# Optimization experiments

Measured on AMD Instinct MI355X. Metric: run time of the kernel, lower is better.

## Reference

```python
import jax, jax.numpy as jnp
import numpy as np

I, H, M, C, LOC, K = 512, 256, 80, 1024, 32, 31
C2 = C // 2
B, S, T = 32, 256, 800


def setup_inputs() -> dict:
    key = jax.random.key(0)
    ks = jax.random.split(key, 20)
    sc = 0.02
    return {
        "encodings": jax.random.normal(ks[0], (B, S, I), jnp.float32),
        "queries": jax.random.normal(ks[1], (B, T, H), jnp.float32),
        "outputs": jax.random.normal(ks[2], (B, T, M), jnp.float32),
        "mask": jnp.ones((B, S), jnp.float32),
        # GRUCell (PyTorch layout: gates ordered r, z, n)
        "w_ih": jax.random.normal(ks[3], (3 * C, I + H), jnp.float32) * sc,
        "w_hh": jax.random.normal(ks[4], (3 * C, C), jnp.float32) * sc,
        "b_ih": jax.random.normal(ks[5], (3 * C,), jnp.float32) * sc,
        "b_hh": jax.random.normal(ks[6], (3 * C,), jnp.float32) * sc,
        "w_q": jax.random.normal(ks[7], (C2, C), jnp.float32) * sc,        # proj_query
        "w_loc1": jax.random.normal(ks[8], (LOC, 1, K), jnp.float32) * sc, # Conv1d(1, loc, K)
        "w_loc2": jax.random.normal(ks[9], (C2, LOC), jnp.float32) * sc,   # Conv1d(loc, C2, 1)
        "w_k": jax.random.normal(ks[10], (C2, I), jnp.float32) * sc,       # proj_key
        "b_k": jax.random.normal(ks[11], (C2,), jnp.float32) * sc,
        "w_agg": jax.random.normal(ks[12], (C2,), jnp.float32) * sc,       # Conv1d(C2, 1, 1)
        "w_t1": jax.random.normal(ks[13], (C, I + C + M), jnp.float32) * sc,
        "b_t1": jax.random.normal(ks[14], (C,), jnp.float32) * sc,
        "w_t2": jax.random.normal(ks[15], (C,), jnp.float32) * sc,
    }


def _conv1d(x, w, pad):
    # x: [B, Cin, S], w: [Cout, Cin, K]
    return jax.lax.conv_general_dilated(
        x, w, window_strides=(1,), padding=[(pad, pad)],
        dimension_numbers=("NCH", "OIH", "NCH"))


def _aligner(encodings, queries, outputs, maskb,
             w_ih, w_hh, b_ih, b_hh, w_q, w_loc1, w_loc2, w_k, b_k,
             w_agg, w_t1, b_t1, w_t2):
    bsize, seqlen, _ = encodings.shape
    # key projection: [B, S, C2]
    key = encodings @ w_k.T + b_k
    h0 = jnp.zeros((bsize, C), encodings.dtype)
    align0 = jnp.full((bsize, seqlen), 1.0 / seqlen, encodings.dtype)
    alpha0 = jnp.zeros((bsize, seqlen), encodings.dtype).at[:, 0].set(1.0)
    trans0 = jnp.full((bsize, 1), 0.5, encodings.dtype)

    def step(carry, xt):
        h, align, trans, alpha = carry
        query, frame = xt  # [B,H], [B,M]
        prev = jnp.einsum("bsi,bs->bi", encodings, alpha)
        x = jnp.concatenate([query, prev], axis=-1)  # [B, H+I]
        gx = x @ w_ih.T + b_ih
        gh = h @ w_hh.T + b_hh
        xr, xz, xn = jnp.split(gx, 3, axis=-1)
        hr, hz, hn = jnp.split(gh, 3, axis=-1)
        r = jax.nn.sigmoid(xr + hr)
        z = jax.nn.sigmoid(xz + hz)
        n = jnp.tanh(xn + r * hn)
        h_new = (1.0 - z) * n + z * h  # GRUCell update
        # location features: [B,1,S] -> [B,LOC,S] -> [B,C2,S]
        loc = _conv1d(align[:, None, :], w_loc1, K // 2)
        loc = jnp.einsum("cl,bls->bcs", w_loc2, loc)
        score = loc + (h_new @ w_q.T)[..., None] + key.swapaxes(1, 2)  # [B,C2,S]
        energy = jnp.einsum("c,bcs->bs", w_agg, jnp.tanh(score))
        energy = jnp.where(maskb, -jnp.inf, energy)
        align_new = jax.nn.softmax(energy, axis=-1)
        shifted = jnp.pad(alpha, ((0, 0), (1, 0)))[:, :-1]  # F.pad(alpha, [1,-1])
        alpha_new = ((1.0 - trans) * alpha + trans * shifted + 1e-7) * align_new
        alpha_new = alpha_new / alpha_new.sum(axis=-1, keepdims=True)
        attend = jnp.einsum("bsi,bs->bi", encodings, alpha_new)
        t_in = jnp.concatenate([attend, frame, h_new], axis=-1)
        t = jax.nn.sigmoid(jnp.tanh(t_in @ w_t1.T + b_t1) @ w_t2[:, None])  # [B,1]
        return (h_new, align_new, t, alpha_new), alpha_new

    xs = (queries.swapaxes(0, 1), outputs.swapaxes(0, 1))
    _, alphas = jax.lax.scan(step, (h0, align0, trans0, alpha0), xs)
    return alphas.swapaxes(0, 1)  # [B, T, S]


def reference(encodings, queries, outputs, mask,
              w_ih, w_hh, b_ih, b_hh, w_q, w_loc1, w_loc2, w_k, b_k,
              w_agg, w_t1, b_t1, w_t2):
    maskb = ~(mask.astype(bool))
    return _aligner(encodings, queries, outputs, maskb,
                    w_ih, w_hh, b_ih, b_hh, w_q, w_loc1, w_loc2, w_k, b_k,
                    w_agg, w_t1, b_t1, w_t2)
```

## Files before the change

kernel.cpp:

```cpp
#include <hip/hip_runtime.h>
#include <cstdint>
#include <cstddef>


namespace cfg {
constexpr int NB = 32, NS = 256, NI = 512, NHq = 256, NM = 80;
constexpr int NC = 1024, NC2 = 512, NT = 800;
constexpr int NBLK = 256, NTHR = 512;

constexpr size_t OFF_KEYT  = 0;
constexpr size_t OFF_WKT   = OFF_KEYT + (size_t)NB * NS * NC2;
constexpr size_t OFF_PU    = OFF_WKT + (size_t)NI * NC2;
constexpr size_t OFF_H     = OFF_PU + (size_t)2 * NB * NI;
constexpr size_t OFF_H16   = OFF_H + (size_t)2 * NC * NB;
constexpr size_t OFF_E     = OFF_H16 + (size_t)NB * NC;
constexpr size_t OFF_W     = OFF_E + (size_t)2 * NB * NS;
constexpr size_t OFF_SE    = OFF_W + (size_t)2 * NB * NS;
constexpr size_t OFF_SW    = OFF_SE + 64;
constexpr size_t OFF_TPART = OFF_SW + 64;
constexpr size_t OFF_TRED  = OFF_TPART + (size_t)NB * NBLK;
constexpr size_t OFF_QBUF  = OFF_TRED + 32;
constexpr size_t OFF_BAR   = OFF_QBUF + (size_t)NB * NC2;
constexpr size_t OFF_Q16   = OFF_BAR + 8192;
constexpr size_t OFF_F16   = OFF_Q16 + (size_t)NT * NB * NHq / 2;
constexpr size_t OFF_WQ16  = OFF_F16 + (size_t)NT * NB * 128 / 2;
constexpr size_t OFF_ENC16 = OFF_WQ16 + (size_t)NC2 * NC / 2;
constexpr size_t WS_FLOATS = OFF_ENC16 + (size_t)NB * NS * NI / 2;
}
using namespace cfg;

typedef __attribute__((ext_vector_type(8))) short short8;
typedef __attribute__((ext_vector_type(4))) float f32x4;

#define MF(a, b, c) __builtin_amdgcn_mfma_f32_16x16x32_bf16((a), (b), (c), 0, 0, 0)
#define LDSC(d, p) asm volatile("global_load_dwordx4 %0, %1, off sc0 sc1" : "=v"(d) : "v"(p))

__device__ __forceinline__ float ld_cg(const float* p) {
  return __hip_atomic_load(p, __ATOMIC_RELAXED, __HIP_MEMORY_SCOPE_AGENT);
}
__device__ __forceinline__ void st_cg(float* p, float v) {
  __hip_atomic_store(p, v, __ATOMIC_RELAXED, __HIP_MEMORY_SCOPE_AGENT);
}
__device__ __forceinline__ void st_cg_u16(unsigned short* p, unsigned short v) {
  asm volatile("global_store_short %0, %1, off sc0 sc1" :: "v"(p), "v"((unsigned)v) : "memory");
}

__device__ __forceinline__ void vw7(short8& a0, short8& a1, short8& a2, short8& a3,
                                    short8& a4, short8& a5, short8& a6) {
  asm volatile("s_waitcnt vmcnt(0)"
               : "+v"(a0), "+v"(a1), "+v"(a2), "+v"(a3), "+v"(a4), "+v"(a5), "+v"(a6));
}
__device__ __forceinline__ void vw8(short8& a0, short8& a1, short8& a2, short8& a3,
                                    short8& a4, short8& a5, short8& a6, short8& a7) {
  asm volatile("s_waitcnt vmcnt(0)"
               : "+v"(a0), "+v"(a1), "+v"(a2), "+v"(a3), "+v"(a4), "+v"(a5), "+v"(a6), "+v"(a7));
}
__device__ __forceinline__ void vw10(short8& a0, short8& a1, short8& a2, short8& a3, short8& a4,
                                     short8& a5, short8& a6, short8& a7, short8& a8, short8& a9) {
  asm volatile("s_waitcnt vmcnt(0)"
               : "+v"(a0), "+v"(a1), "+v"(a2), "+v"(a3), "+v"(a4), "+v"(a5), "+v"(a6),
                 "+v"(a7), "+v"(a8), "+v"(a9));
}
__device__ __forceinline__ void vw15(short8& a0, short8& a1, short8& a2, short8& a3, short8& a4,
                                     short8& a5, short8& a6, short8& a7, short8& a8, short8& a9,
                                     short8& aa, short8& ab2, short8& ac, short8& ad, short8& ae) {
  asm volatile("s_waitcnt vmcnt(0)"
               : "+v"(a0), "+v"(a1), "+v"(a2), "+v"(a3), "+v"(a4), "+v"(a5), "+v"(a6),
                 "+v"(a7), "+v"(a8), "+v"(a9), "+v"(aa), "+v"(ab2), "+v"(ac), "+v"(ad), "+v"(ae));
}
__device__ __forceinline__ void vw16f(f32x4& a0, f32x4& a1, f32x4& a2, f32x4& a3, f32x4& a4,
                                      f32x4& a5, f32x4& a6, f32x4& a7, f32x4& b0, f32x4& b1,
                                      f32x4& b2, f32x4& b3, f32x4& b4, f32x4& b5, f32x4& b6,
                                      f32x4& b7) {
  asm volatile("s_waitcnt vmcnt(0)"
               : "+v"(a0), "+v"(a1), "+v"(a2), "+v"(a3), "+v"(a4), "+v"(a5), "+v"(a6), "+v"(a7),
                 "+v"(b0), "+v"(b1), "+v"(b2), "+v"(b3), "+v"(b4), "+v"(b5), "+v"(b6), "+v"(b7));
}

__device__ __forceinline__ float frcp(float x) {
#if __has_builtin(__builtin_amdgcn_rcpf)
  return __builtin_amdgcn_rcpf(x);
#else
  return 1.f / x;
#endif
}
__device__ __forceinline__ float fsig(float x) { return frcp(1.f + __expf(-x)); }
__device__ __forceinline__ float ftanh(float x) {
  const float e = __expf(2.f * x);
  return 1.f - 2.f * frcp(e + 1.f);
}
__device__ __forceinline__ short f2bf(float f) {
  unsigned u = __float_as_uint(f);
  u += 0x7FFFu + ((u >> 16) & 1u);
  return (short)(u >> 16);
}
__device__ __forceinline__ float bfu(unsigned short u) {
  return __uint_as_float(((unsigned)u) << 16);
}
__device__ __forceinline__ short8 cvt8(f32x4 lo, f32x4 hi) {
  short8 a;
  a[0] = f2bf(lo[0]); a[1] = f2bf(lo[1]); a[2] = f2bf(lo[2]); a[3] = f2bf(lo[3]);
  a[4] = f2bf(hi[0]); a[5] = f2bf(hi[1]); a[6] = f2bf(hi[2]); a[7] = f2bf(hi[3]);
  return a;
}

__device__ __forceinline__ void gbarrier(unsigned* root, unsigned* flags, unsigned& ph) {
  ++ph;
  asm volatile("s_waitcnt vmcnt(0)" ::: "memory");
  __syncthreads();
  unsigned* rootrep = root + 4352;
  if (blockIdx.x == 0) {
    const int t = threadIdx.x;
    if (t > 0 && t < 256) {
      while (__hip_atomic_load(&flags[t * 16], __ATOMIC_RELAXED, __HIP_MEMORY_SCOPE_AGENT) < ph)
        __builtin_amdgcn_s_sleep(1);
    }
    __syncthreads();
    if (t < 32)
      __hip_atomic_store(&rootrep[t * 16], ph, __ATOMIC_RELAXED, __HIP_MEMORY_SCOPE_AGENT);
  } else {
    if (threadIdx.x == 0) {
      __hip_atomic_store(&flags[blockIdx.x * 16], ph, __ATOMIC_RELAXED, __HIP_MEMORY_SCOPE_AGENT);
      while (__hip_atomic_load(&rootrep[(blockIdx.x & 31) * 16], __ATOMIC_RELAXED,
                               __HIP_MEMORY_SCOPE_AGENT) < ph)
        __builtin_amdgcn_s_sleep(1);
    }
  }
  __syncthreads();
}

__device__ __forceinline__ float wcat_val(const float* __restrict__ w_ih,
                                          const float* __restrict__ w_hh,
                                          const float* __restrict__ w_t1,
                                          int kind, int c, int k) {
  if (kind < 3) {
    const int gr = kind * NC + c;
    if (k < 768) return w_ih[(size_t)gr * 768 + k];
    if (k < 1792) return w_hh[(size_t)gr * NC + (k - 768)];
    return 0.f;
  }
  if (k >= 256 && k < 768) return w_t1[(size_t)c * 1616 + (k - 256)];
  if (k >= 768 && k < 1792) return w_t1[(size_t)c * 1616 + 592 + (k - 768)];
  if (k >= 1792 && k < 1872) return w_t1[(size_t)c * 1616 + 512 + (k - 1792)];
  return 0.f;
}

__global__ void k_init(const float* __restrict__ enc, const float* __restrict__ queries,
                       const float* __restrict__ outputs, const float* __restrict__ w_k,
                       const float* __restrict__ w_q, float* __restrict__ ws) {
  const size_t t0 = (size_t)blockIdx.x * blockDim.x + threadIdx.x;
  const size_t gs = (size_t)gridDim.x * blockDim.x;
  for (size_t x = t0; x < (size_t)NI * NC2; x += gs) {
    const int i = (int)(x / NC2), c2 = (int)(x % NC2);
    ws[OFF_WKT + x] = w_k[(size_t)c2 * NI + i];
  }
  for (size_t x = t0; x < (size_t)NB * NI; x += gs) {
    const int b = (int)(x / NI), i = (int)(x % NI);
    ws[OFF_PU + x] = 0.f;
    ws[OFF_PU + (size_t)NB * NI + b * NI + i] = enc[(size_t)b * NS * NI + i];
  }
  for (size_t x = t0; x < (size_t)2 * NC * NB; x += gs) ws[OFF_H + x] = 0.f;
  for (size_t x = t0; x < (size_t)NB * NC; x += gs) ws[OFF_H16 + x] = 0.f;
  for (size_t x = t0; x < (size_t)NB * NS; x += gs) {
    ws[OFF_E + x] = 0.f;
    ws[OFF_E + (size_t)NB * NS + x] = 1.f;
    ws[OFF_W + x] = 0.f;
    ws[OFF_W + (size_t)NB * NS + x] = ((x & (NS - 1)) == 0) ? 1.f : 0.f;
  }
  for (size_t x = t0; x < (size_t)NB; x += gs) {
    ws[OFF_SE + x] = 0.f; ws[OFF_SE + NB + x] = (float)NS;
    ws[OFF_SW + x] = 0.f; ws[OFF_SW + NB + x] = 1.f;
    ws[OFF_TRED + x] = 0.f;
  }
  for (size_t x = t0; x < (size_t)NB * NBLK; x += gs) ws[OFF_TPART + x] = 0.f;
  unsigned* bar = (unsigned*)(ws + OFF_BAR);
  for (size_t x = t0; x < 8192; x += gs) bar[x] = 0u;
  unsigned short* Q16 = (unsigned short*)(ws + OFF_Q16);
  for (size_t x = t0; x < (size_t)NT * NB * NHq; x += gs) {
    const int k = (int)(x & (NHq - 1));
    const int b = (int)((x >> 8) & (NB - 1));
    const int t = (int)(x >> 13);
    Q16[x] = (unsigned short)f2bf(queries[((size_t)b * NT + t) * NHq + k]);
  }
  unsigned short* F16 = (unsigned short*)(ws + OFF_F16);
  for (size_t x = t0; x < (size_t)NT * NB * 128; x += gs) {
    const int k = (int)(x & 127);
    const int b = (int)((x >> 7) & (NB - 1));
    const int t = (int)(x >> 12);
    F16[x] = (k < NM) ? (unsigned short)f2bf(outputs[((size_t)b * NT + t) * NM + k]) : 0;
  }
  unsigned short* WQ16 = (unsigned short*)(ws + OFF_WQ16);
  for (size_t x = t0; x < (size_t)NC2 * NC; x += gs)
    WQ16[x] = (unsigned short)f2bf(w_q[x]);
  unsigned short* ENC16 = (unsigned short*)(ws + OFF_ENC16);
  for (size_t x = t0; x < (size_t)NB * NS * NI; x += gs)
    ENC16[x] = (unsigned short)f2bf(enc[x]);
}

__global__ __launch_bounds__(NTHR) void k_key(const float* __restrict__ enc,
                                              const float* __restrict__ b_k,
                                              float* __restrict__ ws) {
  __shared__ float encl[4 * NI];
  const int bid = blockIdx.x, tid = threadIdx.x;
  const int b = bid >> 3, s0 = (bid & 7) * 32;
  const float* wkT = ws + OFF_WKT;
  float* keyT = ws + OFF_KEYT;
  const float bk = b_k[tid];
  for (int q = 0; q < 8; ++q) {
    const int sb = s0 + q * 4;
    for (int x = tid; x < 4 * NI; x += NTHR) {
      const int ss = x >> 9, i = x & (NI - 1);
      encl[x] = enc[((size_t)(b * NS + sb + ss)) * NI + i];
    }
    __syncthreads();
    float a0 = bk, a1 = bk, a2 = bk, a3 = bk;
    for (int i = 0; i < NI; ++i) {
      const float wv = wkT[(size_t)i * NC2 + tid];
      a0 += wv * encl[i];           a1 += wv * encl[NI + i];
      a2 += wv * encl[2 * NI + i];  a3 += wv * encl[3 * NI + i];
    }
    keyT[((size_t)(b * NS + sb + 0)) * NC2 + tid] = a0;
    keyT[((size_t)(b * NS + sb + 1)) * NC2 + tid] = a1;
    keyT[((size_t)(b * NS + sb + 2)) * NC2 + tid] = a2;
    keyT[((size_t)(b * NS + sb + 3)) * NC2 + tid] = a3;
    __syncthreads();
  }
}

__global__ __launch_bounds__(NTHR, 2) void k_main(
    const float* __restrict__ enc, const float* __restrict__ mask,
    const float* __restrict__ w_ih, const float* __restrict__ w_hh,
    const float* __restrict__ b_ih, const float* __restrict__ b_hh,
    const float* __restrict__ w_loc1, const float* __restrict__ w_loc2,
    const float* __restrict__ w_agg, const float* __restrict__ w_t1,
    const float* __restrict__ b_t1, const float* __restrict__ w_t2,
    float* ws, float* __restrict__ out) {
  const int bid = blockIdx.x, tid = threadIdx.x;
  float* const keyT = ws + OFF_KEYT;
  float* const PU = ws + OFF_PU;
  float* const HB = ws + OFF_H;
  unsigned short* const HB16 = (unsigned short*)(ws + OFF_H16);
  float* const EB = ws + OFF_E;
  float* const WBUF = ws + OFF_W;
  float* const SEB = ws + OFF_SE;
  float* const SWB = ws + OFF_SW;
  float* const TPART = ws + OFF_TPART;
  float* const QBUF = ws + OFF_QBUF;
  unsigned* const root = (unsigned*)(ws + OFF_BAR);
  unsigned* const flags = root + 16;
  unsigned* const qflag = root + 5120;
  unsigned* const rootrep2 = root + 5632;
  const unsigned short* const Q16 = (const unsigned short*)(ws + OFF_Q16);
  const unsigned short* const F16 = (const unsigned short*)(ws + OFF_F16);
  const unsigned short* const WQ16 = (const unsigned short*)(ws + OFF_WQ16);
  const unsigned short* const ENC16 = (const unsigned short*)(ws + OFF_ENC16);

  __shared__ float Cred[2 * 5 * 4 * 64];
  __shared__ float gout2[5 * 4 * 32];
  __shared__ float swinv_l[32];
  __shared__ float tredl[128];
  __shared__ float redT[256];
  __shared__ float alignl[72];
  __shared__ float wl2[34];
  __shared__ float qbl[520];
  __shared__ float Epart[32 * 9];
  __shared__ float wstash[32];
  __shared__ float scal[4];

  const int lane = tid & 63, wv = tid >> 6;
  const int m2 = wv >> 2, k4 = wv & 3;
  const int kg = lane >> 4;
  const int ab = m2 * 16 + (lane & 15);
  const int cs = bid * 4;
  const int pb_b = bid >> 3, pb_s0 = (bid & 7) * 32;
  const int col = lane & 15, quad = lane >> 4;
  unsigned ph = 0;

  short8 wreg[16];
  {
    const int n = lane & 15;
    const int kind = n >> 2, ch = cs + (n & 3);
#pragma unroll
    for (int si = 0; si < 16; ++si) {
      int s = (k4 == 0) ? (si < 8 ? si : (si < 15 ? 16 + si : -1))
            : (k4 == 1) ? 8 + si
            : (k4 == 2) ? (si < 15 ? 31 + si : -1)
                        : (si < 14 ? 46 + si : -1);
      short8 w = {0, 0, 0, 0, 0, 0, 0, 0};
      if (s >= 0) {
        const int k0 = s * 32 + kg * 8;
#pragma unroll
        for (int jj = 0; jj < 8; ++jj)
          w[jj] = f2bf(wcat_val(w_ih, w_hh, w_t1, kind, ch, k0 + jj));
      }
      wreg[si] = w;
    }
  }
  short8 wcA[4];
  unsigned keylo[4][2], keyhi[4][2];
  f32x4 wagr[4];
#pragma unroll
  for (int t = 0; t < 4; ++t) {
    const int mt = 4 * wv + t;
    short8 wfr;
#pragma unroll
    for (int jj = 0; jj < 8; ++jj) {
      const int k = quad * 8 + jj;
      float s = 0.f;
      if (k < 31) {
        const int c2 = mt * 16 + col;
        for (int l = 0; l < 32; ++l) s += w_loc2[c2 * 32 + l] * w_loc1[l * 31 + k];
      }
      wfr[jj] = f2bf(s);
    }
    wcA[t] = wfr;
    const int c2r = mt * 16 + quad * 4;
#pragma unroll
    for (int r = 0; r < 4; ++r) wagr[t][r] = w_agg[c2r + r];
#pragma unroll
    for (int nt = 0; nt < 2; ++nt) {
      const float* kp = &keyT[((size_t)(pb_b * NS + pb_s0 + nt * 16 + col)) * NC2 + c2r];
      keylo[t][nt] = ((unsigned)(unsigned short)f2bf(kp[0])) |
                     (((unsigned)(unsigned short)f2bf(kp[1])) << 16);
      keyhi[t][nt] = ((unsigned)(unsigned short)f2bf(kp[2])) |
                     (((unsigned)(unsigned short)f2bf(kp[3])) << 16);
    }
  }
  if (tid >= 62 && tid < 72) alignl[tid] = 0.f;
  __syncthreads();

  for (int j = 0; j < NT; ++j) {
    const int p = j & 1;
    const float* pu_prev = PU + (size_t)(1 - p) * NB * NI;
    float* pu_cur = PU + (size_t)p * NB * NI;
    const float* h_prev = HB + (size_t)(1 - p) * NC * NB;
    float* h_cur = HB + (size_t)p * NC * NB;
    const unsigned short* hb16_prev = HB16 + (size_t)(1 - p) * NB * NC;
    unsigned short* hb16_cur = HB16 + (size_t)p * NB * NC;
    const float* e_prev = EB + (size_t)(1 - p) * NB * NS;
    float* e_cur = EB + (size_t)p * NB * NS;
    const float* w_prev = WBUF + (size_t)(1 - p) * NB * NS;
    float* w_cur = WBUF + (size_t)p * NB * NS;
    const float* se_prev = SEB + (size_t)(1 - p) * NB;
    float* se_cur = SEB + (size_t)p * NB;
    const float* sw_prev = SWB + (size_t)(1 - p) * NB;
    float* sw_cur = SWB + (size_t)p * NB;

    if (tid < 64) st_cg(&pu_cur[bid * 64 + tid], 0.f);
    if (bid == 0 && tid < NB) st_cg(&se_cur[tid], 0.f);
    if (bid == 1 && tid < NB) st_cg(&sw_cur[tid], 0.f);
    if (tid < NB) swinv_l[tid] = 1.f / ld_cg(&sw_prev[tid]);
    if (tid == 0) scal[0] = ld_cg(&se_prev[pb_b]);
    if (tid < 62) {
      const int sp = pb_s0 + tid - 15;
      alignl[tid] = (sp >= 0 && sp < NS) ? ld_cg(&e_prev[pb_b * NS + sp]) : 0.f;
    }
    if (tid >= 64 && tid < 97) {
      const int i2 = tid - 64, sp = pb_s0 + i2 - 1;
      wl2[i2] = (sp >= 0 && sp < NS) ? ld_cg(&w_prev[pb_b * NS + sp]) : 0.f;
    }
    __syncthreads();

    if (j >= 1 && bid < NB && tid < NS)
      out[((size_t)bid * NT + (j - 1)) * NS + tid] = ld_cg(&w_prev[bid * NS + tid]) * swinv_l[bid];

    f32x4 accA = {0.f, 0.f, 0.f, 0.f}, accB = {0.f, 0.f, 0.f, 0.f};
    if (k4 == 0) {
      const unsigned short* qp = Q16 + ((size_t)j * NB + ab) * NHq + kg * 8;
      const unsigned short* hp = hb16_prev + (size_t)ab * NC + kg * 8;
      short8 h0, h1, h2, h3, h4, h5, h6;
      LDSC(h0, hp);        LDSC(h1, hp + 32);   LDSC(h2, hp + 64);  LDSC(h3, hp + 96);
      LDSC(h4, hp + 128);  LDSC(h5, hp + 160);  LDSC(h6, hp + 192);
      const short8 q0 = *(const short8*)(qp);
      const short8 q1 = *(const short8*)(qp + 32);
      const short8 q2 = *(const short8*)(qp + 64);
      const short8 q3 = *(const short8*)(qp + 96);
      const short8 q4 = *(const short8*)(qp + 128);
      const short8 q5 = *(const short8*)(qp + 160);
      const short8 q6 = *(const short8*)(qp + 192);
      const short8 q7 = *(const short8*)(qp + 224);
      vw7(h0, h1, h2, h3, h4, h5, h6);
      accA = MF(q0, wreg[0], accA); accA = MF(q1, wreg[1], accA);
      accA = MF(q2, wreg[2], accA); accA = MF(q3, wreg[3], accA);
      accA = MF(q4, wreg[4], accA); accA = MF(q5, wreg[5], accA);
      accA = MF(q6, wreg[6], accA); accA = MF(q7, wreg[7], accA);
      accB = MF(h0, wreg[8], accB);  accB = MF(h1, wreg[9], accB);
      accB = MF(h2, wreg[10], accB); accB = MF(h3, wreg[11], accB);
      accB = MF(h4, wreg[12], accB); accB = MF(h5, wreg[13], accB);
      accB = MF(h6, wreg[14], accB);
    } else if (k4 == 1) {
      const float* pp = pu_prev + (size_t)ab * NI + kg * 8;
#pragma unroll
      for (int rd = 0; rd < 2; ++rd) {
        const float* pb = pp + rd * 256;
        f32x4 a0, a1, a2, a3, a4, a5, a6, a7, b0, b1, b2, b3, b4, b5, b6, b7;
        LDSC(a0, pb);        LDSC(b0, pb + 4);
        LDSC(a1, pb + 32);   LDSC(b1, pb + 36);
        LDSC(a2, pb + 64);   LDSC(b2, pb + 68);
        LDSC(a3, pb + 96);   LDSC(b3, pb + 100);
        LDSC(a4, pb + 128);  LDSC(b4, pb + 132);
        LDSC(a5, pb + 160);  LDSC(b5, pb + 164);
        LDSC(a6, pb + 192);  LDSC(b6, pb + 196);
        LDSC(a7, pb + 224);  LDSC(b7, pb + 228);
        vw16f(a0, a1, a2, a3, a4, a5, a6, a7, b0, b1, b2, b3, b4, b5, b6, b7);
        const int w0 = rd * 8;
        accA = MF(cvt8(a0, b0), wreg[w0 + 0], accA);
        accA = MF(cvt8(a1, b1), wreg[w0 + 1], accA);
        accA = MF(cvt8(a2, b2), wreg[w0 + 2], accA);
        accA = MF(cvt8(a3, b3), wreg[w0 + 3], accA);
        accA = MF(cvt8(a4, b4), wreg[w0 + 4], accA);
        accA = MF(cvt8(a5, b5), wreg[w0 + 5], accA);
        accA = MF(cvt8(a6, b6), wreg[w0 + 6], accA);
        accA = MF(cvt8(a7, b7), wreg[w0 + 7], accA);
      }
    } else if (k4 == 2) {
      const unsigned short* hp = hb16_prev + (size_t)ab * NC + kg * 8 + 224;
      short8 h0, h1, h2, h3, h4, h5, h6, h7, h8, h9, ha, hb2, hc, hd, he;
      LDSC(h0, hp);        LDSC(h1, hp + 32);  LDSC(h2, hp + 64);  LDSC(h3, hp + 96);
      LDSC(h4, hp + 128);  LDSC(h5, hp + 160); LDSC(h6, hp + 192); LDSC(h7, hp + 224);
      LDSC(h8, hp + 256);  LDSC(h9, hp + 288); LDSC(ha, hp + 320); LDSC(hb2, hp + 352);
      LDSC(hc, hp + 384);  LDSC(hd, hp + 416); LDSC(he, hp + 448);
      vw15(h0, h1, h2, h3, h4, h5, h6, h7, h8, h9, ha, hb2, hc, hd, he);
      accA = MF(h0, wreg[0], accA);  accA = MF(h1, wreg[1], accA);
      accA = MF(h2, wreg[2], accA);  accA = MF(h3, wreg[3], accA);
      accA = MF(h4, wreg[4], accA);  accA = MF(h5, wreg[5], accA);
      accA = MF(h6, wreg[6], accA);  accA = MF(h7, wreg[7], accA);
      accA = MF(h8, wreg[8], accA);  accA = MF(h9, wreg[9], accA);
      accA = MF(ha, wreg[10], accA); accA = MF(hb2, wreg[11], accA);
      accA = MF(hc, wreg[12], accA); accA = MF(hd, wreg[13], accA);
      accA = MF(he, wreg[14], accA);
    } else {
      const unsigned short* hp = hb16_prev + (size_t)ab * NC + kg * 8 + 704;
      short8 h0, h1, h2, h3, h4, h5, h6, h7, h8, h9;
      LDSC(h0, hp);        LDSC(h1, hp + 32);  LDSC(h2, hp + 64);  LDSC(h3, hp + 96);
      LDSC(h4, hp + 128);  LDSC(h5, hp + 160); LDSC(h6, hp + 192); LDSC(h7, hp + 224);
      LDSC(h8, hp + 256);  LDSC(h9, hp + 288);
      short8 f0 = {0,0,0,0,0,0,0,0}, f1 = f0, f2 = f0, f3 = f0;
      if (j > 0) {
        const unsigned short* fp = F16 + ((size_t)(j - 1) * NB + ab) * 128 + kg * 8;
        f0 = *(const short8*)(fp);
        f1 = *(const short8*)(fp + 32);
        f2 = *(const short8*)(fp + 64);
        f3 = *(const short8*)(fp + 96);
      }
      vw10(h0, h1, h2, h3, h4, h5, h6, h7, h8, h9);
      accA = MF(h0, wreg[0], accA); accA = MF(h1, wreg[1], accA);
      accA = MF(h2, wreg[2], accA); accA = MF(h3, wreg[3], accA);
      accA = MF(h4, wreg[4], accA); accA = MF(h5, wreg[5], accA);
      accA = MF(h6, wreg[6], accA); accA = MF(h7, wreg[7], accA);
      accA = MF(h8, wreg[8], accA); accA = MF(h9, wreg[9], accA);
      accA = MF(f0, wreg[10], accA); accA = MF(f1, wreg[11], accA);
      accA = MF(f2, wreg[12], accA); accA = MF(f3, wreg[13], accA);
    }
    {
      auto cidx = [](int m, int sg, int r, int l) { return ((m * 5 + sg) * 4 + r) * 64 + l; };
      if (k4 == 0) {
#pragma unroll
        for (int r = 0; r < 4; ++r) {
          Cred[cidx(m2, 0, r, lane)] = accA[r];
          Cred[cidx(m2, 1, r, lane)] = accB[r];
        }
      } else {
        const int sg = 1 + k4;
#pragma unroll
        for (int r = 0; r < 4; ++r) Cred[cidx(m2, sg, r, lane)] = accA[r];
      }
    }
    __syncthreads();
    {
      const int n = tid & 15, b = tid >> 4;
      const int m2r = b >> 4, bm = b & 15, l = (bm >> 2) * 16 + n, r = bm & 3;
      auto cidx = [](int m, int sg, int rr, int ll) { return ((m * 5 + sg) * 4 + rr) * 64 + ll; };
      const float s0 = Cred[cidx(m2r, 0, r, l)];
      const float sB = Cred[cidx(m2r, 1, r, l)];
      const float s1 = Cred[cidx(m2r, 2, r, l)];
      const float s2 = sB + Cred[cidx(m2r, 3, r, l)] + Cred[cidx(m2r, 4, r, l)];
      const float swv = swinv_l[b];
      const int kind = n >> 2, c4o = n & 3;
      if (kind == 2) {
        gout2[2 * 128 + c4o * 32 + b] = s0 + swv * s1;
        gout2[3 * 128 + c4o * 32 + b] = s2;
      } else {
        const int slot = (kind == 3) ? 4 : kind;
        gout2[slot * 128 + c4o * 32 + b] = s0 + swv * s1 + s2;
      }
    }
    __syncthreads();
    if (tid < 128) {
      const int c4o = tid >> 5, b = tid & 31, c = cs + c4o;
      const float xr = gout2[0 * 128 + c4o * 32 + b] + b_ih[c] + b_hh[c];
      const float xz = gout2[1 * 128 + c4o * 32 + b] + b_ih[NC + c] + b_hh[NC + c];
      const float xn = gout2[2 * 128 + c4o * 32 + b] + b_ih[2 * NC + c];
      const float hn = gout2[3 * 128 + c4o * 32 + b] + b_hh[2 * NC + c];
      const float tp = gout2[4 * 128 + c4o * 32 + b];
      const float r = fsig(xr), z = fsig(xz);
      const float nn = ftanh(xn + r * hn);
      const float hnew = (1.f - z) * nn + z * h_prev[c * 32 + b];
      h_cur[c * 32 + b] = hnew;
      st_cg_u16(&hb16_cur[(size_t)b * NC + c], (unsigned short)f2bf(hnew));
      tredl[c4o * 32 + b] = w_t2[c] * ftanh(tp + b_t1[c]);
    }
    __syncthreads();
    if (tid < NB)
      st_cg(&TPART[(size_t)tid * NBLK + bid],
            tredl[tid] + tredl[32 + tid] + tredl[64 + tid] + tredl[96 + tid]);
    gbarrier(root, flags, ph);

    const float tpv = (tid < 256) ? ld_cg(&TPART[(size_t)pb_b * NBLK + tid]) : 0.f;

    if (bid < 32) {
      f32x4 qacc = {0.f, 0.f, 0.f, 0.f};
      const unsigned short* hb = hb16_cur + (size_t)ab * NC + kg * 8;
      short8 g0, g1, g2, g3, g4, g5, g6, g7;
      LDSC(g0, hb + (k4 * 8 + 0) * 32); LDSC(g1, hb + (k4 * 8 + 1) * 32);
      LDSC(g2, hb + (k4 * 8 + 2) * 32); LDSC(g3, hb + (k4 * 8 + 3) * 32);
      LDSC(g4, hb + (k4 * 8 + 4) * 32); LDSC(g5, hb + (k4 * 8 + 5) * 32);
      LDSC(g6, hb + (k4 * 8 + 6) * 32); LDSC(g7, hb + (k4 * 8 + 7) * 32);
      const int jq = bid * 16 + col;
      const unsigned short* wp = WQ16 + (size_t)jq * NC + k4 * 8 * 32 + kg * 8;
      vw8(g0, g1, g2, g3, g4, g5, g6, g7);
      qacc = MF(g0, *(const short8*)(wp), qacc);
      qacc = MF(g1, *(const short8*)(wp + 32), qacc);
      qacc = MF(g2, *(const short8*)(wp + 64), qacc);
      qacc = MF(g3, *(const short8*)(wp + 96), qacc);
      qacc = MF(g4, *(const short8*)(wp + 128), qacc);
      qacc = MF(g5, *(const short8*)(wp + 160), qacc);
      qacc = MF(g6, *(const short8*)(wp + 192), qacc);
      qacc = MF(g7, *(const short8*)(wp + 224), qacc);
#pragma unroll
      for (int r = 0; r < 4; ++r) Cred[((m2 * 4 + k4) * 4 + r) * 64 + lane] = qacc[r];
      __syncthreads();
      {
        const int col2 = tid & 15, b2 = tid >> 4;
        const int m2r = b2 >> 4, bm = b2 & 15, l = (bm >> 2) * 16 + col2, r = bm & 3;
        float s = 0.f;
#pragma unroll
        for (int kk = 0; kk < 4; ++kk) s += Cred[((m2r * 4 + kk) * 4 + r) * 64 + l];
        st_cg(&QBUF[(size_t)b2 * NC2 + bid * 16 + col2], s);
      }
      asm volatile("s_waitcnt vmcnt(0)" ::: "memory");
      __syncthreads();
      if (tid == 0)
        __hip_atomic_store(&qflag[bid * 16], (unsigned)(j + 1),
                           __ATOMIC_RELAXED, __HIP_MEMORY_SCOPE_AGENT);
    }

    if (tid < 256) redT[tid] = tpv;
    __syncthreads();
    if (tid < 64) {
      float s = redT[tid] + redT[tid + 64] + redT[tid + 128] + redT[tid + 192];
#pragma unroll
      for (int off = 32; off > 0; off >>= 1) s += __shfl_xor(s, off);
      if (tid == 0) scal[2] = s;
    }
    f32x4 bacc[2][4];
    {
      const float invSE = 1.f / scal[0];
#pragma unroll
      for (int nt = 0; nt < 2; ++nt) {
        const int base = nt * 16 + col + quad * 8;
        short8 bv;
#pragma unroll
        for (int jj = 0; jj < 8; ++jj) bv[jj] = f2bf(alignl[base + jj] * invSE);
#pragma unroll
        for (int t = 0; t < 4; ++t) {
          f32x4 acc;
          acc[0] = __uint_as_float(keylo[t][nt] << 16);
          acc[1] = __uint_as_float(keylo[t][nt] & 0xffff0000u);
          acc[2] = __uint_as_float(keyhi[t][nt] << 16);
          acc[3] = __uint_as_float(keyhi[t][nt] & 0xffff0000u);
          bacc[nt][t] = MF(wcA[t], bv, acc);
        }
      }
    }
    if (bid == 128) {
      if (tid < 32) {
        while (__hip_atomic_load(&qflag[tid * 16], __ATOMIC_RELAXED,
                                 __HIP_MEMORY_SCOPE_AGENT) < (unsigned)(j + 1))
          __builtin_amdgcn_s_sleep(1);
      }
      __syncthreads();
      if (tid < 32)
        __hip_atomic_store(&rootrep2[tid * 16], (unsigned)(j + 1),
                           __ATOMIC_RELAXED, __HIP_MEMORY_SCOPE_AGENT);
    } else {
      if (tid == 0) {
        while (__hip_atomic_load(&rootrep2[(bid & 31) * 16], __ATOMIC_RELAXED,
                                 __HIP_MEMORY_SCOPE_AGENT) < (unsigned)(j + 1))
          __builtin_amdgcn_s_sleep(1);
      }
    }
    __syncthreads();

    {
      const int b = pb_b, s0v = pb_s0;
      qbl[tid] = ld_cg(&QBUF[(size_t)b * NC2 + tid]);
      __syncthreads();
      const float invSW = swinv_l[b];
      const float tr = (j == 0) ? 0.5f : fsig(scal[2]);
#pragma unroll
      for (int nt = 0; nt < 2; ++nt) {
        float pe = 0.f;
#pragma unroll
        for (int t = 0; t < 4; ++t) {
          const int c2b = (4 * wv + t) * 16 + quad * 4;
          const f32x4 av = bacc[nt][t];
          pe += wagr[t][0] * ftanh(av[0] + qbl[c2b + 0]);
          pe += wagr[t][1] * ftanh(av[1] + qbl[c2b + 1]);
          pe += wagr[t][2] * ftanh(av[2] + qbl[c2b + 2]);
          pe += wagr[t][3] * ftanh(av[3] + qbl[c2b + 3]);
        }
        pe += __shfl_xor(pe, 16);
        pe += __shfl_xor(pe, 32);
        if (lane < 16) Epart[(nt * 16 + col) * 9 + wv] = pe;
      }
      __syncthreads();
      if (tid < 32) {
        const int sl = tid, s = s0v + sl;
        float Ev = 0.f;
#pragma unroll
        for (int w8 = 0; w8 < 8; ++w8) Ev += Epart[sl * 9 + w8];
        const float ev = (mask[b * NS + s] != 0.f) ? __expf(Ev) : 0.f;
        const float csv = ((1.f - tr) * wl2[sl + 1] + tr * wl2[sl]) * invSW + 1e-7f;
        const float wvv = csv * ev;
        st_cg(&e_cur[b * NS + s], ev);
        st_cg(&w_cur[b * NS + s], wvv);
        wstash[sl] = wvv;
        float se = ev, sw2 = wvv;
#pragma unroll
        for (int off = 16; off > 0; off >>= 1) {
          se += __shfl_down(se, off, 32);
          sw2 += __shfl_down(sw2, off, 32);
        }
        if (sl == 0) { atomicAdd(&se_cur[b], se); atomicAdd(&sw_cur[b], sw2); }
      }
      __syncthreads();
      {
        const unsigned short* ep = ENC16 + ((size_t)(b * NS + s0v)) * NI + tid;
        float acc = 0.f;
#pragma unroll 8
        for (int ss = 0; ss < 32; ++ss) acc += wstash[ss] * bfu(ep[(size_t)ss * NI]);
        atomicAdd(&pu_cur[(size_t)b * NI + tid], acc);
      }
    }
    gbarrier(root, flags, ph);
  }

  if (bid < NB && tid < NS) {
    const float invSW = 1.f / ld_cg(&SWB[NB + bid]);
    out[((size_t)bid * NT + (NT - 1)) * NS + tid] =
        ld_cg(&WBUF[(size_t)NB * NS + bid * NS + tid]) * invSW;
  }
}

extern "C" void kernel_launch(void* const* d_in, const int* in_sizes, int n_in,
                              void* d_out, int out_size, void* d_ws, size_t ws_size,
                              hipStream_t stream) {
  const float* enc     = (const float*)d_in[0];
  const float* queries = (const float*)d_in[1];
  const float* outputs = (const float*)d_in[2];
  const float* mask    = (const float*)d_in[3];
  const float* w_ih    = (const float*)d_in[4];
  const float* w_hh    = (const float*)d_in[5];
  const float* b_ih    = (const float*)d_in[6];
  const float* b_hh    = (const float*)d_in[7];
  const float* w_q     = (const float*)d_in[8];
  const float* w_loc1  = (const float*)d_in[9];
  const float* w_loc2  = (const float*)d_in[10];
  const float* w_k     = (const float*)d_in[11];
  const float* b_k     = (const float*)d_in[12];
  const float* w_agg   = (const float*)d_in[13];
  const float* w_t1    = (const float*)d_in[14];
  const float* b_t1    = (const float*)d_in[15];
  const float* w_t2    = (const float*)d_in[16];
  float* ws = (float*)d_ws;
  float* out = (float*)d_out;
  (void)in_sizes; (void)n_in; (void)out_size; (void)ws_size;

  k_init<<<dim3(1024), dim3(256), 0, stream>>>(enc, queries, outputs, w_k, w_q, ws);
  k_key<<<dim3(NBLK), dim3(NTHR), 0, stream>>>(enc, b_k, ws);
  k_main<<<dim3(NBLK), dim3(NTHR), 0, stream>>>(enc, mask, w_ih, w_hh, b_ih, b_hh,
                                                w_loc1, w_loc2, w_agg, w_t1,
                                                b_t1, w_t2, ws, out);
}
```

Before: 20.34 ms.

## Hoist next-step GRU hidden MFMAs before grid barrier to overlap with sync

Splits the per-step GRU gate MFMA work so the hidden-state and query portions (k4 != 1) for step j+1 are computed at the end of step j, before the grid-wide barrier wait. Only the attention-context portion (k4 == 1), which depends on data produced after the barrier, stays at the top of the loop. This is meant to take the hidden-state matmul off the critical path after each barrier. It also drops the occupancy hint from 2 to 1 blocks per CU so the accumulators held across the barrier have more registers. Correctness depends on the new hidden state being complete and visible at the point where the early MFMAs read it.

```diff
diff --git a/kernel.cpp b/kernel.cpp
--- a/kernel.cpp
+++ b/kernel.cpp
@@ -227,7 +227,7 @@
   }
 }
 
-__global__ __launch_bounds__(NTHR, 2) void k_main(
+__global__ __launch_bounds__(NTHR, 1) void k_main(
     const float* __restrict__ enc, const float* __restrict__ mask,
     const float* __restrict__ w_ih, const float* __restrict__ w_hh,
     const float* __restrict__ b_ih, const float* __restrict__ b_hh,
@@ -329,45 +329,11 @@
   if (tid >= 62 && tid < 72) alignl[tid] = 0.f;
   __syncthreads();
 
-  for (int j = 0; j < NT; ++j) {
-    const int p = j & 1;
-    const float* pu_prev = PU + (size_t)(1 - p) * NB * NI;
-    float* pu_cur = PU + (size_t)p * NB * NI;
-    const float* h_prev = HB + (size_t)(1 - p) * NC * NB;
-    float* h_cur = HB + (size_t)p * NC * NB;
-    const unsigned short* hb16_prev = HB16 + (size_t)(1 - p) * NB * NC;
-    unsigned short* hb16_cur = HB16 + (size_t)p * NB * NC;
-    const float* e_prev = EB + (size_t)(1 - p) * NB * NS;
-    float* e_cur = EB + (size_t)p * NB * NS;
-    const float* w_prev = WBUF + (size_t)(1 - p) * NB * NS;
-    float* w_cur = WBUF + (size_t)p * NB * NS;
-    const float* se_prev = SEB + (size_t)(1 - p) * NB;
-    float* se_cur = SEB + (size_t)p * NB;
-    const float* sw_prev = SWB + (size_t)(1 - p) * NB;
-    float* sw_cur = SWB + (size_t)p * NB;
-
-    if (tid < 64) st_cg(&pu_cur[bid * 64 + tid], 0.f);
-    if (bid == 0 && tid < NB) st_cg(&se_cur[tid], 0.f);
-    if (bid == 1 && tid < NB) st_cg(&sw_cur[tid], 0.f);
-    if (tid < NB) swinv_l[tid] = 1.f / ld_cg(&sw_prev[tid]);
-    if (tid == 0) scal[0] = ld_cg(&se_prev[pb_b]);
-    if (tid < 62) {
-      const int sp = pb_s0 + tid - 15;
-      alignl[tid] = (sp >= 0 && sp < NS) ? ld_cg(&e_prev[pb_b * NS + sp]) : 0.f;
-    }
-    if (tid >= 64 && tid < 97) {
-      const int i2 = tid - 64, sp = pb_s0 + i2 - 1;
-      wl2[i2] = (sp >= 0 && sp < NS) ? ld_cg(&w_prev[pb_b * NS + sp]) : 0.f;
-    }
-    __syncthreads();
-
-    if (j >= 1 && bid < NB && tid < NS)
-      out[((size_t)bid * NT + (j - 1)) * NS + tid] = ld_cg(&w_prev[bid * NS + tid]) * swinv_l[bid];
-
-    f32x4 accA = {0.f, 0.f, 0.f, 0.f}, accB = {0.f, 0.f, 0.f, 0.f};
+  auto gru_mfma = [&](int jj, const unsigned short* hbp, f32x4& oA, f32x4& oB) {
+    f32x4 aA = {0.f, 0.f, 0.f, 0.f}, aB = {0.f, 0.f, 0.f, 0.f};
     if (k4 == 0) {
-      const unsigned short* qp = Q16 + ((size_t)j * NB + ab) * NHq + kg * 8;
-      const unsigned short* hp = hb16_prev + (size_t)ab * NC + kg * 8;
+      const unsigned short* qp = Q16 + ((size_t)jj * NB + ab) * NHq + kg * 8;
+      const unsigned short* hp = hbp + (size_t)ab * NC + kg * 8;
       short8 h0, h1, h2, h3, h4, h5, h6;
       LDSC(h0, hp);        LDSC(h1, hp + 32);   LDSC(h2, hp + 64);  LDSC(h3, hp + 96);
       LDSC(h4, hp + 128);  LDSC(h5, hp + 160);  LDSC(h6, hp + 192);
@@ -380,15 +346,95 @@
       const short8 q6 = *(const short8*)(qp + 192);
       const short8 q7 = *(const short8*)(qp + 224);
       vw7(h0, h1, h2, h3, h4, h5, h6);
-      accA = MF(q0, wreg[0], accA); accA = MF(q1, wreg[1], accA);
-      accA = MF(q2, wreg[2], accA); accA = MF(q3, wreg[3], accA);
-      accA = MF(q4, wreg[4], accA); accA = MF(q5, wreg[5], accA);
-      accA = MF(q6, wreg[6], accA); accA = MF(q7, wreg[7], accA);
-      accB = MF(h0, wreg[8], accB);  accB = MF(h1, wreg[9], accB);
-      accB = MF(h2, wreg[10], accB); accB = MF(h3, wreg[11], accB);
-      accB = MF(h4, wreg[12], accB); accB = MF(h5, wreg[13], accB);
-      accB = MF(h6, wreg[14], accB);
-    } else if (k4 == 1) {
+      aA = MF(q0, wreg[0], aA); aA = MF(q1, wreg[1], aA);
+      aA = MF(q2, wreg[2], aA); aA = MF(q3, wreg[3], aA);
+      aA = MF(q4, wreg[4], aA); aA = MF(q5, wreg[5], aA);
+      aA = MF(q6, wreg[6], aA); aA = MF(q7, wreg[7], aA);
+      aB = MF(h0, wreg[8], aB);  aB = MF(h1, wreg[9], aB);
+      aB = MF(h2, wreg[10], aB); aB = MF(h3, wreg[11], aB);
+      aB = MF(h4, wreg[12], aB); aB = MF(h5, wreg[13], aB);
+      aB = MF(h6, wreg[14], aB);
+    } else if (k4 == 2) {
+      const unsigned short* hp = hbp + (size_t)ab * NC + kg * 8 + 224;
+      short8 h0, h1, h2, h3, h4, h5, h6, h7, h8, h9, ha, hb2, hc, hd, he;
+      LDSC(h0, hp);        LDSC(h1, hp + 32);  LDSC(h2, hp + 64);  LDSC(h3, hp + 96);
+      LDSC(h4, hp + 128);  LDSC(h5, hp + 160); LDSC(h6, hp + 192); LDSC(h7, hp + 224);
+      LDSC(h8, hp + 256);  LDSC(h9, hp + 288); LDSC(ha, hp + 320); LDSC(hb2, hp + 352);
+      LDSC(hc, hp + 384);  LDSC(hd, hp + 416); LDSC(he, hp + 448);
+      vw15(h0, h1, h2, h3, h4, h5, h6, h7, h8, h9, ha, hb2, hc, hd, he);
+      aA = MF(h0, wreg[0], aA);  aA = MF(h1, wreg[1], aA);
+      aA = MF(h2, wreg[2], aA);  aA = MF(h3, wreg[3], aA);
+      aA = MF(h4, wreg[4], aA);  aA = MF(h5, wreg[5], aA);
+      aA = MF(h6, wreg[6], aA);  aA = MF(h7, wreg[7], aA);
+      aA = MF(h8, wreg[8], aA);  aA = MF(h9, wreg[9], aA);
+      aA = MF(ha, wreg[10], aA); aA = MF(hb2, wreg[11], aA);
+      aA = MF(hc, wreg[12], aA); aA = MF(hd, wreg[13], aA);
+      aA = MF(he, wreg[14], aA);
+    } else {
+      const unsigned short* hp = hbp + (size_t)ab * NC + kg * 8 + 704;
+      short8 h0, h1, h2, h3, h4, h5, h6, h7, h8, h9;
+      LDSC(h0, hp);        LDSC(h1, hp + 32);  LDSC(h2, hp + 64);  LDSC(h3, hp + 96);
+      LDSC(h4, hp + 128);  LDSC(h5, hp + 160); LDSC(h6, hp + 192); LDSC(h7, hp + 224);
+      LDSC(h8, hp + 256);  LDSC(h9, hp + 288);
+      short8 f0 = {0,0,0,0,0,0,0,0}, f1 = f0, f2 = f0, f3 = f0;
+      if (jj > 0) {
+        const unsigned short* fp = F16 + ((size_t)(jj - 1) * NB + ab) * 128 + kg * 8;
+        f0 = *(const short8*)(fp);
+        f1 = *(const short8*)(fp + 32);
+        f2 = *(const short8*)(fp + 64);
+        f3 = *(const short8*)(fp + 96);
+      }
+      vw10(h0, h1, h2, h3, h4, h5, h6, h7, h8, h9);
+      aA = MF(h0, wreg[0], aA); aA = MF(h1, wreg[1], aA);
+      aA = MF(h2, wreg[2], aA); aA = MF(h3, wreg[3], aA);
+      aA = MF(h4, wreg[4], aA); aA = MF(h5, wreg[5], aA);
+      aA = MF(h6, wreg[6], aA); aA = MF(h7, wreg[7], aA);
+      aA = MF(h8, wreg[8], aA); aA = MF(h9, wreg[9], aA);
+      aA = MF(f0, wreg[10], aA); aA = MF(f1, wreg[11], aA);
+      aA = MF(f2, wreg[12], aA); aA = MF(f3, wreg[13], aA);
+    }
+    oA = aA; oB = aB;
+  };
+
+  f32x4 accA = {0.f, 0.f, 0.f, 0.f}, accB = {0.f, 0.f, 0.f, 0.f};
+  if (k4 != 1) gru_mfma(0, HB16 + (size_t)NB * NC, accA, accB);
+
+  for (int j = 0; j < NT; ++j) {
+    const int p = j & 1;
+    const float* pu_prev = PU + (size_t)(1 - p) * NB * NI;
+    float* pu_cur = PU + (size_t)p * NB * NI;
+    const float* h_prev = HB + (size_t)(1 - p) * NC * NB;
+    float* h_cur = HB + (size_t)p * NC * NB;
+    unsigned short* hb16_cur = HB16 + (size_t)p * NB * NC;
+    const float* e_prev = EB + (size_t)(1 - p) * NB * NS;
+    float* e_cur = EB + (size_t)p * NB * NS;
+    const float* w_prev = WBUF + (size_t)(1 - p) * NB * NS;
+    float* w_cur = WBUF + (size_t)p * NB * NS;
+    const float* se_prev = SEB + (size_t)(1 - p) * NB;
+    float* se_cur = SEB + (size_t)p * NB;
+    const float* sw_prev = SWB + (size_t)(1 - p) * NB;
+    float* sw_cur = SWB + (size_t)p * NB;
+
+    if (tid < 64) st_cg(&pu_cur[bid * 64 + tid], 0.f);
+    if (bid == 0 && tid < NB) st_cg(&se_cur[tid], 0.f);
+    if (bid == 1 && tid < NB) st_cg(&sw_cur[tid], 0.f);
+    if (tid < NB) swinv_l[tid] = 1.f / ld_cg(&sw_prev[tid]);
+    if (tid == 0) scal[0] = ld_cg(&se_prev[pb_b]);
+    if (tid < 62) {
+      const int sp = pb_s0 + tid - 15;
+      alignl[tid] = (sp >= 0 && sp < NS) ? ld_cg(&e_prev[pb_b * NS + sp]) : 0.f;
+    }
+    if (tid >= 64 && tid < 97) {
+      const int i2 = tid - 64, sp = pb_s0 + i2 - 1;
+      wl2[i2] = (sp >= 0 && sp < NS) ? ld_cg(&w_prev[pb_b * NS + sp]) : 0.f;
+    }
+    __syncthreads();
+
+    if (j >= 1 && bid < NB && tid < NS)
+      out[((size_t)bid * NT + (j - 1)) * NS + tid] = ld_cg(&w_prev[bid * NS + tid]) * swinv_l[bid];
+
+    if (k4 == 1) {
+      accA = (f32x4){0.f, 0.f, 0.f, 0.f};
       const float* pp = pu_prev + (size_t)ab * NI + kg * 8;
 #pragma unroll
       for (int rd = 0; rd < 2; ++rd) {
@@ -413,44 +459,6 @@
         accA = MF(cvt8(a6, b6), wreg[w0 + 6], accA);
         accA = MF(cvt8(a7, b7), wreg[w0 + 7], accA);
       }
-    } else if (k4 == 2) {
-      const unsigned short* hp = hb16_prev + (size_t)ab * NC + kg * 8 + 224;
-      short8 h0, h1, h2, h3, h4, h5, h6, h7, h8, h9, ha, hb2, hc, hd, he;
-      LDSC(h0, hp);        LDSC(h1, hp + 32);  LDSC(h2, hp + 64);  LDSC(h3, hp + 96);
-      LDSC(h4, hp + 128);  LDSC(h5, hp + 160); LDSC(h6, hp + 192); LDSC(h7, hp + 224);
-      LDSC(h8, hp + 256);  LDSC(h9, hp + 288); LDSC(ha, hp + 320); LDSC(hb2, hp + 352);
-      LDSC(hc, hp + 384);  LDSC(hd, hp + 416); LDSC(he, hp + 448);
-      vw15(h0, h1, h2, h3, h4, h5, h6, h7, h8, h9, ha, hb2, hc, hd, he);
-      accA = MF(h0, wreg[0], accA);  accA = MF(h1, wreg[1], accA);
-      accA = MF(h2, wreg[2], accA);  accA = MF(h3, wreg[3], accA);
-      accA = MF(h4, wreg[4], accA);  accA = MF(h5, wreg[5], accA);
-      accA = MF(h6, wreg[6], accA);  accA = MF(h7, wreg[7], accA);
-      accA = MF(h8, wreg[8], accA);  accA = MF(h9, wreg[9], accA);
-      accA = MF(ha, wreg[10], accA); accA = MF(hb2, wreg[11], accA);
-      accA = MF(hc, wreg[12], accA); accA = MF(hd, wreg[13], accA);
-      accA = MF(he, wreg[14], accA);
-    } else {
-      const unsigned short* hp = hb16_prev + (size_t)ab * NC + kg * 8 + 704;
-      short8 h0, h1, h2, h3, h4, h5, h6, h7, h8, h9;
-      LDSC(h0, hp);        LDSC(h1, hp + 32);  LDSC(h2, hp + 64);  LDSC(h3, hp + 96);
-      LDSC(h4, hp + 128);  LDSC(h5, hp + 160); LDSC(h6, hp + 192); LDSC(h7, hp + 224);
-      LDSC(h8, hp + 256);  LDSC(h9, hp + 288);
-      short8 f0 = {0,0,0,0,0,0,0,0}, f1 = f0, f2 = f0, f3 = f0;
-      if (j > 0) {
-        const unsigned short* fp = F16 + ((size_t)(j - 1) * NB + ab) * 128 + kg * 8;
-        f0 = *(const short8*)(fp);
-        f1 = *(const short8*)(fp + 32);
-        f2 = *(const short8*)(fp + 64);
-        f3 = *(const short8*)(fp + 96);
-      }
-      vw10(h0, h1, h2, h3, h4, h5, h6, h7, h8, h9);
-      accA = MF(h0, wreg[0], accA); accA = MF(h1, wreg[1], accA);
-      accA = MF(h2, wreg[2], accA); accA = MF(h3, wreg[3], accA);
-      accA = MF(h4, wreg[4], accA); accA = MF(h5, wreg[5], accA);
-      accA = MF(h6, wreg[6], accA); accA = MF(h7, wreg[7], accA);
-      accA = MF(h8, wreg[8], accA); accA = MF(h9, wreg[9], accA);
-      accA = MF(f0, wreg[10], accA); accA = MF(f1, wreg[11], accA);
-      accA = MF(f2, wreg[12], accA); accA = MF(f3, wreg[13], accA);
     }
     {
       auto cidx = [](int m, int sg, int r, int l) { return ((m * 5 + sg) * 4 + r) * 64 + l; };
@@ -573,6 +581,8 @@
         }
       }
     }
+    if (k4 != 1 && j + 1 < NT) gru_mfma(j + 1, hb16_cur, accA, accB);
+
     if (bid == 128) {
       if (tid < 32) {
         while (__hip_atomic_load(&qflag[tid * 16], __ATOMIC_RELAXED,
```

Measured after the change: 23.74 ms. +16.7%, slower.

## Replace grid barrier and Q-flag relay with tagged data-flag handoff

Applied to the files above, without the earlier changes.

Removes the full grid barrier after the transition partial sums and the two-level qflag/rootrep2 relay. Only the 32 query-projection blocks now wait, polling per-block flags with vectorized loads. They reduce the transition sum themselves and publish query values and the transition scalar as self-tagged 16-byte records that consumer blocks poll directly. The output store is moved later so it overlaps the wait. This trades a global barrier for finer dependencies, at the cost of more polling traffic and correctness that depends on the 16-byte stores being seen atomically.

```diff
diff --git a/kernel.cpp b/kernel.cpp
--- a/kernel.cpp
+++ b/kernel.cpp
@@ -25,15 +25,21 @@
 constexpr size_t OFF_F16   = OFF_Q16 + (size_t)NT * NB * NHq / 2;
 constexpr size_t OFF_WQ16  = OFF_F16 + (size_t)NT * NB * 128 / 2;
 constexpr size_t OFF_ENC16 = OFF_WQ16 + (size_t)NC2 * NC / 2;
-constexpr size_t WS_FLOATS = OFF_ENC16 + (size_t)NB * NS * NI / 2;
+constexpr size_t OFF_QT    = OFF_ENC16 + (size_t)NB * NS * NI / 2;
+constexpr size_t OFF_TRC   = OFF_QT + 24576;
+constexpr size_t WS_FLOATS = OFF_TRC + 128;
 }
 using namespace cfg;
 
 typedef __attribute__((ext_vector_type(8))) short short8;
 typedef __attribute__((ext_vector_type(4))) float f32x4;
+typedef __attribute__((ext_vector_type(4))) unsigned u32x4;
 
 #define MF(a, b, c) __builtin_amdgcn_mfma_f32_16x16x32_bf16((a), (b), (c), 0, 0, 0)
 #define LDSC(d, p) asm volatile("global_load_dwordx4 %0, %1, off sc0 sc1" : "=v"(d) : "v"(p))
+#define LDSC4W(d, p) asm volatile("global_load_dwordx4 %0, %1, off sc0 sc1\n\ts_waitcnt vmcnt(0)" \
+                                  : "=v"(d) : "v"(p))
+#define STSC4(p, d) asm volatile("global_store_dwordx4 %0, %1, off sc0 sc1" :: "v"(p), "v"(d) : "memory")
 
 __device__ __forceinline__ float ld_cg(const float* p) {
   return __hip_atomic_load(p, __ATOMIC_RELAXED, __HIP_MEMORY_SCOPE_AGENT);
@@ -175,6 +181,8 @@
   for (size_t x = t0; x < (size_t)NB * NBLK; x += gs) ws[OFF_TPART + x] = 0.f;
   unsigned* bar = (unsigned*)(ws + OFF_BAR);
   for (size_t x = t0; x < 8192; x += gs) bar[x] = 0u;
+  unsigned* qt = (unsigned*)(ws + OFF_QT);
+  for (size_t x = t0; x < 24576 + 128; x += gs) qt[x] = 0u;
   unsigned short* Q16 = (unsigned short*)(ws + OFF_Q16);
   for (size_t x = t0; x < (size_t)NT * NB * NHq; x += gs) {
     const int k = (int)(x & (NHq - 1));
@@ -245,11 +253,11 @@
   float* const SEB = ws + OFF_SE;
   float* const SWB = ws + OFF_SW;
   float* const TPART = ws + OFF_TPART;
-  float* const QBUF = ws + OFF_QBUF;
   unsigned* const root = (unsigned*)(ws + OFF_BAR);
   unsigned* const flags = root + 16;
-  unsigned* const qflag = root + 5120;
-  unsigned* const rootrep2 = root + 5632;
+  unsigned* const hfl = root + 5120;
+  unsigned* const qt = (unsigned*)(ws + OFF_QT);
+  unsigned* const trc = (unsigned*)(ws + OFF_TRC);
   const unsigned short* const Q16 = (const unsigned short*)(ws + OFF_Q16);
   const unsigned short* const F16 = (const unsigned short*)(ws + OFF_F16);
   const unsigned short* const WQ16 = (const unsigned short*)(ws + OFF_WQ16);
@@ -345,6 +353,7 @@
     float* se_cur = SEB + (size_t)p * NB;
     const float* sw_prev = SWB + (size_t)(1 - p) * NB;
     float* sw_cur = SWB + (size_t)p * NB;
+    const unsigned tag = (unsigned)(j + 1);
 
     if (tid < 64) st_cg(&pu_cur[bid * 64 + tid], 0.f);
     if (bid == 0 && tid < NB) st_cg(&se_cur[tid], 0.f);
@@ -360,9 +369,6 @@
       wl2[i2] = (sp >= 0 && sp < NS) ? ld_cg(&w_prev[pb_b * NS + sp]) : 0.f;
     }
     __syncthreads();
-
-    if (j >= 1 && bid < NB && tid < NS)
-      out[((size_t)bid * NT + (j - 1)) * NS + tid] = ld_cg(&w_prev[bid * NS + tid]) * swinv_l[bid];
 
     f32x4 accA = {0.f, 0.f, 0.f, 0.f}, accB = {0.f, 0.f, 0.f, 0.f};
     if (k4 == 0) {
@@ -504,11 +510,23 @@
     if (tid < NB)
       st_cg(&TPART[(size_t)tid * NBLK + bid],
             tredl[tid] + tredl[32 + tid] + tredl[64 + tid] + tredl[96 + tid]);
-    gbarrier(root, flags, ph);
-
-    const float tpv = (tid < 256) ? ld_cg(&TPART[(size_t)pb_b * NBLK + tid]) : 0.f;
+    asm volatile("s_waitcnt vmcnt(0)" ::: "memory");
+    __syncthreads();
+    if (tid == 0)
+      __hip_atomic_store(&hfl[bid], tag, __ATOMIC_RELAXED, __HIP_MEMORY_SCOPE_AGENT);
 
     if (bid < 32) {
+      if (tid < 64) {
+        const unsigned* pp = hfl + tid * 4;
+        for (;;) {
+          u32x4 v;
+          LDSC4W(v, pp);
+          if (v[0] >= tag && v[1] >= tag && v[2] >= tag && v[3] >= tag) break;
+          __builtin_amdgcn_s_sleep(4);
+        }
+      }
+      __syncthreads();
+      if (tid < 256) redT[tid] = ld_cg(&TPART[(size_t)bid * NBLK + tid]);
       f32x4 qacc = {0.f, 0.f, 0.f, 0.f};
       const unsigned short* hb = hb16_cur + (size_t)ab * NC + kg * 8;
       short8 g0, g1, g2, g3, g4, g5, g6, g7;
@@ -536,23 +554,34 @@
         float s = 0.f;
 #pragma unroll
         for (int kk = 0; kk < 4; ++kk) s += Cred[((m2r * 4 + kk) * 4 + r) * 64 + l];
-        st_cg(&QBUF[(size_t)b2 * NC2 + bid * 16 + col2], s);
-      }
-      asm volatile("s_waitcnt vmcnt(0)" ::: "memory");
+        qbl[b2 * 16 + col2] = s;
+        if (tid < 64) {
+          float t = redT[tid] + redT[tid + 64] + redT[tid + 128] + redT[tid + 192];
+#pragma unroll
+          for (int off = 32; off > 0; off >>= 1) t += __shfl_xor(t, off);
+          if (tid == 0) scal[3] = t;
+        }
+      }
       __syncthreads();
-      if (tid == 0)
-        __hip_atomic_store(&qflag[bid * 16], (unsigned)(j + 1),
-                           __ATOMIC_RELAXED, __HIP_MEMORY_SCOPE_AGENT);
-    }
-
-    if (tid < 256) redT[tid] = tpv;
-    __syncthreads();
-    if (tid < 64) {
-      float s = redT[tid] + redT[tid + 64] + redT[tid + 128] + redT[tid + 192];
-#pragma unroll
-      for (int off = 32; off > 0; off >>= 1) s += __shfl_xor(s, off);
-      if (tid == 0) scal[2] = s;
-    }
+      if (tid < 192) {
+        const int b2 = tid / 6, k = tid % 6, c0 = k * 3;
+        u32x4 v;
+        v[0] = __float_as_uint(qbl[b2 * 16 + c0]);
+        v[1] = (k < 5) ? __float_as_uint(qbl[b2 * 16 + c0 + 1]) : 0u;
+        v[2] = (k < 5) ? __float_as_uint(qbl[b2 * 16 + c0 + 2]) : 0u;
+        v[3] = tag;
+        STSC4(qt + ((size_t)(b2 * 32 + bid) * 6 + k) * 4, v);
+      } else if (tid == 192) {
+        u32x4 v;
+        v[0] = __float_as_uint(scal[3]); v[1] = 0u; v[2] = 0u; v[3] = tag;
+        STSC4(trc + (size_t)bid * 4, v);
+      }
+      __syncthreads();
+    }
+
+    if (j >= 1 && bid < NB && tid < NS)
+      out[((size_t)bid * NT + (j - 1)) * NS + tid] = ld_cg(&w_prev[bid * NS + tid]) * swinv_l[bid];
+
     f32x4 bacc[2][4];
     {
       const float invSE = 1.f / scal[0];
@@ -573,29 +602,31 @@
         }
       }
     }
-    if (bid == 128) {
-      if (tid < 32) {
-        while (__hip_atomic_load(&qflag[tid * 16], __ATOMIC_RELAXED,
-                                 __HIP_MEMORY_SCOPE_AGENT) < (unsigned)(j + 1))
-          __builtin_amdgcn_s_sleep(1);
-      }
-      __syncthreads();
-      if (tid < 32)
-        __hip_atomic_store(&rootrep2[tid * 16], (unsigned)(j + 1),
-                           __ATOMIC_RELAXED, __HIP_MEMORY_SCOPE_AGENT);
-    } else {
-      if (tid == 0) {
-        while (__hip_atomic_load(&rootrep2[(bid & 31) * 16], __ATOMIC_RELAXED,
-                                 __HIP_MEMORY_SCOPE_AGENT) < (unsigned)(j + 1))
-          __builtin_amdgcn_s_sleep(1);
+    if (tid < 193) {
+      const unsigned* pp = (tid < 192)
+          ? qt + ((size_t)(pb_b * 32 + tid / 6) * 6 + (tid % 6)) * 4
+          : trc + (size_t)pb_b * 4;
+      u32x4 v;
+      for (;;) {
+        LDSC4W(v, pp);
+        if (v[3] >= tag) break;
+        __builtin_amdgcn_s_sleep(2);
+      }
+      if (tid < 192) {
+        const int g = tid / 6, k = tid % 6, c0 = g * 16 + k * 3;
+        qbl[c0] = __uint_as_float(v[0]);
+        if (k < 5) {
+          qbl[c0 + 1] = __uint_as_float(v[1]);
+          qbl[c0 + 2] = __uint_as_float(v[2]);
+        }
+      } else {
+        scal[2] = __uint_as_float(v[0]);
       }
     }
     __syncthreads();
 
     {
       const int b = pb_b, s0v = pb_s0;
-      qbl[tid] = ld_cg(&QBUF[(size_t)b * NC2 + tid]);
-      __syncthreads();
       const float invSW = swinv_l[b];
       const float tr = (j == 0) ? 0.5f : fsig(scal[2]);
 #pragma unroll
```

After: 19.29 ms. 5.2% less time.
